# Kernel optimization log

Measured on AMD Instinct MI355X. Metric: run time of the kernel, lower is better.

## Reference

```python
import jax, jax.numpy as jnp
import numpy as np

B, T, IN, EH, GH = 256, 512, 128, 512, 512  # batch, time, channels, enc hidden, gen hidden
UPDATE_BIAS = 1.0
CLIP_VAL = 5.0


def setup_inputs() -> dict:
    key = jax.random.key(0)
    ks = jax.random.split(key, 7)
    s = 0.05  # weight scale to keep gates unsaturated
    return {
        "src": jax.random.normal(ks[0], (B, T, IN), jnp.float32),
        "eps": jax.random.normal(ks[1], (B, GH), jnp.float32),  # reparam noise for generator IC
        "enc_Wi": jax.random.normal(ks[2], (3 * EH, IN), jnp.float32) * s,   # torch GRU weight_ih_l0 (r,z,n)
        "enc_Wh": jax.random.normal(ks[3], (3 * EH, EH), jnp.float32) * s,   # torch GRU weight_hh_l0
        "enc2gen_W": jax.random.normal(ks[4], (2 * GH, EH), jnp.float32) * s,  # Linear enc_state -> ic params
        "gen_Wh_ru": jax.random.normal(ks[5], (2 * GH, GH), jnp.float32) * s,  # GruCellModified fc_h_ru
        "gen_W_rhc": jax.random.normal(ks[6], (GH, GH), jnp.float32) * s,      # GruCellModified fc_rh_c
    }


def _forward(src, eps, enc_Wi, enc_Wh, enc2gen_W, gen_Wh_ru, gen_W_rhc):
    b, t, _ = src.shape
    H = enc_Wh.shape[1]
    # ---- encoder: standard GRU (bias=False), batch_first, 1 layer, unidirectional ----
    xW = jnp.einsum('bti,ki->tbk', src, enc_Wi)  # [T,B,3H], input projections hoisted out of scan

    def enc_step(h, xw):
        gh = h @ enc_Wh.T  # [B,3H]
        xr, xz, xn = jnp.split(xw, 3, axis=-1)
        hr, hz, hn = jnp.split(gh, 3, axis=-1)
        r = jax.nn.sigmoid(xr + hr)
        z = jax.nn.sigmoid(xz + hz)
        n = jnp.tanh(xn + r * hn)
        h_new = (1.0 - z) * n + z * h
        return h_new, None

    h0 = jnp.zeros((b, H), src.dtype)
    enc_last, _ = jax.lax.scan(enc_step, h0, xW)  # [B,EH]

    # ---- enc2gen Linear -> generator IC distribution params ----
    ic_params = enc_last @ enc2gen_W.T  # [B, 2*GH]
    mu, lv = jnp.split(ic_params, 2, axis=1)
    ic = mu + jnp.exp(0.5 * lv) * eps  # reparameterized sample, [B,GH]

    # ---- generator: GruCellModified recurrence, input_size=0 (no input term) ----
    def gen_step(h, _):
        ru = h @ gen_Wh_ru.T  # [B,2*GH]
        r, u = jnp.split(ru, 2, axis=-1)
        r = jax.nn.sigmoid(r)
        u = jax.nn.sigmoid(u + UPDATE_BIAS)  # forced update-gate bias
        c = jnp.tanh((r * h) @ gen_W_rhc.T)
        h_new = u * h + (1.0 - u) * c
        return h_new, h_new

    _, gen_hidden = jax.lax.scan(gen_step, ic, None, length=t)  # [T,B,GH]
    gen_out = jnp.clip(gen_hidden.transpose(1, 0, 2), -CLIP_VAL, CLIP_VAL)  # [B,T,GH]
    return gen_out, ic_params


def reference(src, eps, enc_Wi, enc_Wh, enc2gen_W, gen_Wh_ru, gen_W_rhc):
    return _forward(src, eps, enc_Wi, enc_Wh, enc2gen_W, gen_Wh_ru, gen_W_rhc)
```

## Files before the change

kernel.cpp:

```cpp
#include <hip/hip_runtime.h>
#include <hip/hip_bf16.h>
#include <math.h>

#define BB 256
#define TT 512
#define INW 128
#define EH 512
#define GH 512

#define NGB 32
#define NGRP 8
#define MG 32
#define NB 16

typedef __attribute__((ext_vector_type(8))) short bf16x8;
typedef __attribute__((ext_vector_type(4))) float f32x4;
typedef __attribute__((ext_vector_type(2))) unsigned long long u64x2;

__device__ __forceinline__ float sigm(float x){ return 1.0f/(1.0f+__expf(-x)); }
__device__ __forceinline__ short f2bf(float x){
    __hip_bfloat16 h = __float2bfloat16(x);
    return *reinterpret_cast<short*>(&h);
}

__device__ __forceinline__ unsigned long long ld_coh64(const unsigned long long* p){
    return __hip_atomic_load(p, __ATOMIC_RELAXED, __HIP_MEMORY_SCOPE_AGENT);
}
__device__ __forceinline__ void st_coh32(unsigned* p, unsigned v){
    __hip_atomic_store(p, v, __ATOMIC_RELAXED, __HIP_MEMORY_SCOPE_AGENT);
}

__device__ __forceinline__ void grp_sync(unsigned* cnt, unsigned target) {
    asm volatile("s_waitcnt vmcnt(0)" ::: "memory");
    __syncthreads();
    if (threadIdx.x == 0) {
        __hip_atomic_fetch_add(cnt, 1u, __ATOMIC_RELAXED, __HIP_MEMORY_SCOPE_AGENT);
        long spins = 0;
        while (__hip_atomic_load(cnt, __ATOMIC_RELAXED, __HIP_MEMORY_SCOPE_AGENT) < target) {
            __builtin_amdgcn_s_sleep(1);
            if (++spins > (1L << 22)) break;
        }
    }
    __syncthreads();
}

__device__ __forceinline__ void pack_store_bf(unsigned* dst_even, short bv, int l15){
    unsigned mine = (unsigned short)bv;
    unsigned othr = __shfl_xor(mine, 1);
    if (!(l15 & 1)) st_coh32(dst_even, (othr << 16) | mine);
}

__global__ __launch_bounds__(512, 1) void enc_kernel(
    const float* __restrict__ src,
    const float* __restrict__ Wi,
    const float* __restrict__ Wh,
    short*       __restrict__ hbf,
    float*       __restrict__ hencf,
    unsigned*    __restrict__ bars)
{
    __shared__ __align__(16) char sH[32*1024];
    __shared__ __align__(16) char sX[32*256];
    __shared__ float sR[32*17];
    __shared__ float sZ[32*17];
    __shared__ float sHfp[32*17];

    const int bid = blockIdx.x;
    const int g = bid / NGB, ng = bid % NGB;
    const int tid = threadIdx.x;
    const int wid = tid >> 6, lane = tid & 63;
    const int l15 = lane & 15, lk = lane >> 4;
    const int j0 = ng * NB;
    const int b0 = g * MG;
    unsigned* cnt = bars + g * 32;

    bf16x8 whB[16], wxB[4];
    if (wid < 6) {
        const int gate = wid >> 1;
        const float* wrh = Wh + (size_t)(gate*EH + j0 + l15) * EH;
        const float* wrx = Wi + (size_t)(gate*EH + j0 + l15) * INW;
        #pragma unroll
        for (int kt = 0; kt < 16; ++kt) {
            int ke = kt*32 + lk*8;
            float4 f0 = *(const float4*)(wrh + ke);
            float4 f1 = *(const float4*)(wrh + ke + 4);
            bf16x8 v;
            v[0]=f2bf(f0.x); v[1]=f2bf(f0.y); v[2]=f2bf(f0.z); v[3]=f2bf(f0.w);
            v[4]=f2bf(f1.x); v[5]=f2bf(f1.y); v[6]=f2bf(f1.z); v[7]=f2bf(f1.w);
            whB[kt] = v;
        }
        #pragma unroll
        for (int kt = 0; kt < 4; ++kt) {
            int ke = kt*32 + lk*8;
            float4 f0 = *(const float4*)(wrx + ke);
            float4 f1 = *(const float4*)(wrx + ke + 4);
            bf16x8 v;
            v[0]=f2bf(f0.x); v[1]=f2bf(f0.y); v[2]=f2bf(f0.z); v[3]=f2bf(f0.w);
            v[4]=f2bf(f1.x); v[5]=f2bf(f1.y); v[6]=f2bf(f1.z); v[7]=f2bf(f1.w);
            wxB[kt] = v;
        }
    }
    {
        int row = tid >> 4, col = tid & 15;
        sHfp[row*17 + col] = 0.0f;
    }

    for (int t = 0; t < TT; ++t) {
        const short* hsrc = hbf + (size_t)(t & 1) * BB * EH;
        short*       hdst = hbf + (size_t)((t + 1) & 1) * BB * EH;

        #pragma unroll
        for (int i = 0; i < 4; ++i) {
            int row = i*8 + wid;
            int kb  = lane << 4;
            const unsigned long long* gp =
                (const unsigned long long*)((const char*)(hsrc + (size_t)(b0 + row)*EH) + kb);
            unsigned long long v0 = ld_coh64(gp);
            unsigned long long v1 = ld_coh64(gp + 1);
            u64x2 v; v[0] = v0; v[1] = v1;
            *(u64x2*)(sH + row*1024 + (kb ^ ((row & 7) << 4))) = v;
        }
        {
            int e = tid * 8;
            int row = e >> 7, k = e & 127;
            const float* sp = src + ((size_t)(b0 + row)*TT + t)*INW + k;
            float4 f0 = *(const float4*)sp;
            float4 f1 = *(const float4*)(sp + 4);
            bf16x8 v;
            v[0]=f2bf(f0.x); v[1]=f2bf(f0.y); v[2]=f2bf(f0.z); v[3]=f2bf(f0.w);
            v[4]=f2bf(f1.x); v[5]=f2bf(f1.y); v[6]=f2bf(f1.z); v[7]=f2bf(f1.w);
            int kb = (k*2) ^ ((row & 7) << 4);
            *(bf16x8*)(sX + row*256 + kb) = v;
        }
        __syncthreads();

        f32x4 acch = {0.f,0.f,0.f,0.f};
        f32x4 accx = {0.f,0.f,0.f,0.f};
        const int m = wid & 1;
        if (wid < 6) {
            const int arow = m*16 + l15;
            const int asw  = (arow & 7) << 4;
            const char* hb = sH + arow*1024;
            const char* xb = sX + arow*256;
            #pragma unroll
            for (int kt = 0; kt < 16; ++kt) {
                int kb = kt*64 + lk*16;
                bf16x8 a = *(const bf16x8*)(hb + (kb ^ asw));
                acch = __builtin_amdgcn_mfma_f32_16x16x32_bf16(a, whB[kt], acch, 0, 0, 0);
            }
            #pragma unroll
            for (int kt = 0; kt < 4; ++kt) {
                int kb = kt*64 + lk*16;
                bf16x8 a = *(const bf16x8*)(xb + (kb ^ asw));
                accx = __builtin_amdgcn_mfma_f32_16x16x32_bf16(a, wxB[kt], accx, 0, 0, 0);
            }
        }
        if (wid < 2) {
            #pragma unroll
            for (int v = 0; v < 4; ++v) {
                int row = m*16 + lk*4 + v;
                sR[row*17 + l15] = sigm(accx[v] + acch[v]);
            }
        } else if (wid < 4) {
            #pragma unroll
            for (int v = 0; v < 4; ++v) {
                int row = m*16 + lk*4 + v;
                sZ[row*17 + l15] = sigm(accx[v] + acch[v]);
            }
        }
        __syncthreads();
        if (wid == 4 || wid == 5) {
            #pragma unroll
            for (int v = 0; v < 4; ++v) {
                int row = m*16 + lk*4 + v;
                float r  = sR[row*17 + l15];
                float z  = sZ[row*17 + l15];
                float n  = tanhf(accx[v] + r * acch[v]);
                float hp = sHfp[row*17 + l15];
                float hn = (1.f - z)*n + z*hp;
                sHfp[row*17 + l15] = hn;
                unsigned* dst = (unsigned*)&hdst[(size_t)(b0 + row)*EH + j0 + (l15 & ~1)];
                pack_store_bf(dst, f2bf(hn), l15);
                if (t == TT - 1) hencf[(size_t)(b0 + row)*EH + j0 + l15] = hn;
            }
        }
        grp_sync(cnt, (unsigned)((t + 1) * NGB));
    }
}

__global__ __launch_bounds__(256) void ic_kernel(
    const float* __restrict__ henc,
    const float* __restrict__ W,
    const float* __restrict__ eps,
    float*       __restrict__ out_icp,
    float*       __restrict__ gh0f,
    short*       __restrict__ gh0b)
{
    __shared__ float hb[EH];
    const int b = blockIdx.x, tid = threadIdx.x;
    for (int k = tid; k < EH; k += 256) hb[k] = henc[(size_t)b*EH + k];
    __syncthreads();

    for (int jj = tid; jj < GH; jj += 256) {
        const float4* wm = (const float4*)(W + (size_t)jj * EH);
        const float4* wl = (const float4*)(W + (size_t)(GH + jj) * EH);
        float am = 0.f, al = 0.f;
        #pragma unroll 4
        for (int k4 = 0; k4 < EH/4; ++k4) {
            float4 h = ((const float4*)hb)[k4];
            float4 a = wm[k4], c = wl[k4];
            am += h.x*a.x + h.y*a.y + h.z*a.z + h.w*a.w;
            al += h.x*c.x + h.y*c.y + h.z*c.z + h.w*c.w;
        }
        out_icp[(size_t)b*2*GH + jj]      = am;
        out_icp[(size_t)b*2*GH + GH + jj] = al;
        float icv = am + __expf(0.5f * al) * eps[(size_t)b*GH + jj];
        gh0f[(size_t)b*GH + jj] = icv;
        gh0b[(size_t)b*GH + jj] = f2bf(icv);
    }
}

__global__ __launch_bounds__(512, 1) void gen_kernel(
    const float* __restrict__ Wru,
    const float* __restrict__ Wc,
    const float* __restrict__ gh0f,
    short*       __restrict__ hbf,
    short*       __restrict__ rhbf,
    float*       __restrict__ out,
    unsigned*    __restrict__ bars)
{
    __shared__ __align__(16) char sH[32*1024];
    __shared__ float sU[32*17];
    __shared__ float sHfp[32*17];

    const int bid = blockIdx.x;
    const int g = bid / NGB, ng = bid % NGB;
    const int tid = threadIdx.x;
    const int wid = tid >> 6, lane = tid & 63;
    const int l15 = lane & 15, lk = lane >> 4;
    const int j0 = ng * NB;
    const int b0 = g * MG;
    unsigned* cnt = bars + g * 32;
    short* rhg = rhbf + (size_t)g * MG * GH;

    bf16x8 wB[16];
    if (wid < 6) {
        const float* wr;
        if (wid < 2)      wr = Wru + (size_t)(j0 + l15) * GH;
        else if (wid < 4) wr = Wru + (size_t)(GH + j0 + l15) * GH;
        else              wr = Wc  + (size_t)(j0 + l15) * GH;
        #pragma unroll
        for (int kt = 0; kt < 16; ++kt) {
            int ke = kt*32 + lk*8;
            float4 f0 = *(const float4*)(wr + ke);
            float4 f1 = *(const float4*)(wr + ke + 4);
            bf16x8 v;
            v[0]=f2bf(f0.x); v[1]=f2bf(f0.y); v[2]=f2bf(f0.z); v[3]=f2bf(f0.w);
            v[4]=f2bf(f1.x); v[5]=f2bf(f1.y); v[6]=f2bf(f1.z); v[7]=f2bf(f1.w);
            wB[kt] = v;
        }
    }
    {
        int row = tid >> 4, col = tid & 15;
        sHfp[row*17 + col] = gh0f[(size_t)(b0 + row)*GH + j0 + col];
    }

    for (int t = 0; t < TT; ++t) {
        const short* hsrc = hbf + (size_t)(t & 1) * BB * GH;
        short*       hdst = hbf + (size_t)((t + 1) & 1) * BB * GH;

        #pragma unroll
        for (int i = 0; i < 4; ++i) {
            int row = i*8 + wid;
            int kb  = lane << 4;
            const unsigned long long* gp =
                (const unsigned long long*)((const char*)(hsrc + (size_t)(b0 + row)*GH) + kb);
            unsigned long long v0 = ld_coh64(gp);
            unsigned long long v1 = ld_coh64(gp + 1);
            u64x2 v; v[0] = v0; v[1] = v1;
            *(u64x2*)(sH + row*1024 + (kb ^ ((row & 7) << 4))) = v;
        }
        __syncthreads();

        if (wid < 4) {
            const int m = wid & 1;
            const int arow = m*16 + l15;
            const int asw  = (arow & 7) << 4;
            const char* hb = sH + arow*1024;
            f32x4 acc = {0.f,0.f,0.f,0.f};
            #pragma unroll
            for (int kt = 0; kt < 16; ++kt) {
                int kb = kt*64 + lk*16;
                bf16x8 a = *(const bf16x8*)(hb + (kb ^ asw));
                acc = __builtin_amdgcn_mfma_f32_16x16x32_bf16(a, wB[kt], acc, 0, 0, 0);
            }
            if (wid < 2) {
                #pragma unroll
                for (int v = 0; v < 4; ++v) {
                    int row = m*16 + lk*4 + v;
                    float hp = sHfp[row*17 + l15];
                    float rv = sigm(acc[v]);
                    unsigned* dst = (unsigned*)&rhg[(size_t)row*GH + j0 + (l15 & ~1)];
                    pack_store_bf(dst, f2bf(rv * hp), l15);
                }
            } else {
                #pragma unroll
                for (int v = 0; v < 4; ++v) {
                    int row = m*16 + lk*4 + v;
                    sU[row*17 + l15] = sigm(acc[v] + 1.0f);
                }
            }
        }
        grp_sync(cnt, (unsigned)((2*t + 1) * NGB));

        #pragma unroll
        for (int i = 0; i < 4; ++i) {
            int row = i*8 + wid;
            int kb  = lane << 4;
            const unsigned long long* gp =
                (const unsigned long long*)((const char*)(rhg + (size_t)row*GH) + kb);
            unsigned long long v0 = ld_coh64(gp);
            unsigned long long v1 = ld_coh64(gp + 1);
            u64x2 v; v[0] = v0; v[1] = v1;
            *(u64x2*)(sH + row*1024 + (kb ^ ((row & 7) << 4))) = v;
        }
        __syncthreads();

        if (wid == 4 || wid == 5) {
            const int m = wid & 1;
            const int arow = m*16 + l15;
            const int asw  = (arow & 7) << 4;
            const char* hb = sH + arow*1024;
            f32x4 acc = {0.f,0.f,0.f,0.f};
            #pragma unroll
            for (int kt = 0; kt < 16; ++kt) {
                int kb = kt*64 + lk*16;
                bf16x8 a = *(const bf16x8*)(hb + (kb ^ asw));
                acc = __builtin_amdgcn_mfma_f32_16x16x32_bf16(a, wB[kt], acc, 0, 0, 0);
            }
            #pragma unroll
            for (int v = 0; v < 4; ++v) {
                int row = m*16 + lk*4 + v;
                float cv = tanhf(acc[v]);
                float u  = sU[row*17 + l15];
                float hp = sHfp[row*17 + l15];
                float hn = u*hp + (1.0f - u)*cv;
                sHfp[row*17 + l15] = hn;
                unsigned* dst = (unsigned*)&hdst[(size_t)(b0 + row)*GH + j0 + (l15 & ~1)];
                pack_store_bf(dst, f2bf(hn), l15);
                out[((size_t)(b0 + row)*TT + t)*GH + j0 + l15] = fminf(fmaxf(hn, -5.0f), 5.0f);
            }
        }
        grp_sync(cnt, (unsigned)((2*t + 2) * NGB));
    }
}

extern "C" void kernel_launch(void* const* d_in, const int* in_sizes, int n_in,
                              void* d_out, int out_size, void* d_ws, size_t ws_size,
                              hipStream_t stream) {
    (void)in_sizes; (void)n_in; (void)out_size; (void)ws_size;

    const float* src    = (const float*)d_in[0];
    const float* eps    = (const float*)d_in[1];
    const float* enc_Wi = (const float*)d_in[2];
    const float* enc_Wh = (const float*)d_in[3];
    const float* e2g    = (const float*)d_in[4];
    const float* gWru   = (const float*)d_in[5];
    const float* gWc    = (const float*)d_in[6];
    float* out = (float*)d_out;

    char* ws = (char*)d_ws;
    unsigned* bars = (unsigned*)ws;
    float* hencf = (float*)(ws + 8192);
    float* gh0f  = (float*)(ws + 8192 + 512*1024);
    short* encH  = (short*)(ws + 8192 + 1024*1024);
    short* genH  = (short*)(ws + 8192 + 1536*1024);
    short* rhbf  = (short*)(ws + 8192 + 2048*1024);

    hipMemsetAsync(bars, 0, 8192, stream);
    hipMemsetAsync(encH, 0, (size_t)BB*EH*2, stream);

    enc_kernel<<<dim3(256), dim3(512), 0, stream>>>(src, enc_Wi, enc_Wh, encH, hencf, bars);
    ic_kernel <<<dim3(256), dim3(256), 0, stream>>>(hencf, e2g, eps,
                                                    out + (size_t)BB*TT*GH, gh0f, genH);
    gen_kernel<<<dim3(256), dim3(512), 0, stream>>>(gWru, gWc, gh0f, genH, rhbf, out,
                                                    bars + 1024);
}
```

Before: 5.691 ms.

## Regroup blocks into 16-block groups and use per-block flag barriers

Changes the partition from 8 groups of 32 blocks (32 batch rows, 16 columns each) to 16 groups of 16 blocks (16 batch rows, 32 columns each), so each grid barrier spans fewer blocks and each block loads half as much shared hidden state per step. The atomic-counter barrier is replaced with per-block epoch flags that one wavefront polls in parallel with __all, without sleeping. The MFMA K loop is also split across two accumulators to shorten the dependency chain. The risks are heavier weight-register load per block, busy polling traffic without sleep, and a smaller spin-limit fallback.

```diff
diff --git a/kernel.cpp b/kernel.cpp
--- a/kernel.cpp
+++ b/kernel.cpp
@@ -8,10 +8,11 @@
 #define EH 512
 #define GH 512
 
-#define NGB 32
-#define NGRP 8
-#define MG 32
-#define NB 16
+#define NGRP 16
+#define NGB 16
+#define MG 16
+#define NB 32
+#define FLS 16
 
 typedef __attribute__((ext_vector_type(8))) short bf16x8;
 typedef __attribute__((ext_vector_type(4))) float f32x4;
@@ -30,15 +31,17 @@
     __hip_atomic_store(p, v, __ATOMIC_RELAXED, __HIP_MEMORY_SCOPE_AGENT);
 }
 
-__device__ __forceinline__ void grp_sync(unsigned* cnt, unsigned target) {
+__device__ __forceinline__ void grp_barrier(unsigned* gf, int ng, unsigned e){
     asm volatile("s_waitcnt vmcnt(0)" ::: "memory");
     __syncthreads();
-    if (threadIdx.x == 0) {
-        __hip_atomic_fetch_add(cnt, 1u, __ATOMIC_RELAXED, __HIP_MEMORY_SCOPE_AGENT);
+    if (threadIdx.x == 0) st_coh32(gf + ng*FLS, e);
+    if (threadIdx.x < 64) {
+        const unsigned* p = gf + (threadIdx.x & (NGB-1)) * FLS;
         long spins = 0;
-        while (__hip_atomic_load(cnt, __ATOMIC_RELAXED, __HIP_MEMORY_SCOPE_AGENT) < target) {
-            __builtin_amdgcn_s_sleep(1);
-            if (++spins > (1L << 22)) break;
+        for (;;) {
+            unsigned v = __hip_atomic_load(p, __ATOMIC_RELAXED, __HIP_MEMORY_SCOPE_AGENT);
+            if (__all((int)(v >= e))) break;
+            if (++spins > (1L << 20)) break;
         }
     }
     __syncthreads();
@@ -56,28 +59,29 @@
     const float* __restrict__ Wh,
     short*       __restrict__ hbf,
     float*       __restrict__ hencf,
-    unsigned*    __restrict__ bars)
+    unsigned*    __restrict__ flags)
 {
-    __shared__ __align__(16) char sH[32*1024];
-    __shared__ __align__(16) char sX[32*256];
-    __shared__ float sR[32*17];
-    __shared__ float sZ[32*17];
-    __shared__ float sHfp[32*17];
+    __shared__ __align__(16) char sH[MG*1024];
+    __shared__ __align__(16) char sX[MG*256];
+    __shared__ float sR[MG*33];
+    __shared__ float sZ[MG*33];
+    __shared__ float sHfp[MG*33];
 
     const int bid = blockIdx.x;
-    const int g = bid / NGB, ng = bid % NGB;
+    const int g = bid >> 4, ng = bid & 15;
     const int tid = threadIdx.x;
     const int wid = tid >> 6, lane = tid & 63;
     const int l15 = lane & 15, lk = lane >> 4;
     const int j0 = ng * NB;
     const int b0 = g * MG;
-    unsigned* cnt = bars + g * 32;
+    unsigned* gf = flags + g * NGB * FLS;
 
     bf16x8 whB[16], wxB[4];
+    const int gate = wid >> 1, ct = wid & 1;
+    const int col = ct*16 + l15;
     if (wid < 6) {
-        const int gate = wid >> 1;
-        const float* wrh = Wh + (size_t)(gate*EH + j0 + l15) * EH;
-        const float* wrx = Wi + (size_t)(gate*EH + j0 + l15) * INW;
+        const float* wrh = Wh + (size_t)(gate*EH + j0 + col) * EH;
+        const float* wrx = Wi + (size_t)(gate*EH + j0 + col) * INW;
         #pragma unroll
         for (int kt = 0; kt < 16; ++kt) {
             int ke = kt*32 + lk*8;
@@ -99,19 +103,17 @@
             wxB[kt] = v;
         }
     }
-    {
-        int row = tid >> 4, col = tid & 15;
-        sHfp[row*17 + col] = 0.0f;
-    }
+    sHfp[(tid >> 5)*33 + (tid & 31)] = 0.0f;
 
     for (int t = 0; t < TT; ++t) {
         const short* hsrc = hbf + (size_t)(t & 1) * BB * EH;
         short*       hdst = hbf + (size_t)((t + 1) & 1) * BB * EH;
 
         #pragma unroll
-        for (int i = 0; i < 4; ++i) {
-            int row = i*8 + wid;
-            int kb  = lane << 4;
+        for (int i = 0; i < 2; ++i) {
+            int c = i*512 + tid;
+            int row = c >> 6;
+            int kb  = (c & 63) << 4;
             const unsigned long long* gp =
                 (const unsigned long long*)((const char*)(hsrc + (size_t)(b0 + row)*EH) + kb);
             unsigned long long v0 = ld_coh64(gp);
@@ -119,33 +121,35 @@
             u64x2 v; v[0] = v0; v[1] = v1;
             *(u64x2*)(sH + row*1024 + (kb ^ ((row & 7) << 4))) = v;
         }
-        {
-            int e = tid * 8;
-            int row = e >> 7, k = e & 127;
+        if (tid < 256) {
+            int row = tid >> 4, k = (tid & 15) * 8;
             const float* sp = src + ((size_t)(b0 + row)*TT + t)*INW + k;
             float4 f0 = *(const float4*)sp;
             float4 f1 = *(const float4*)(sp + 4);
             bf16x8 v;
             v[0]=f2bf(f0.x); v[1]=f2bf(f0.y); v[2]=f2bf(f0.z); v[3]=f2bf(f0.w);
             v[4]=f2bf(f1.x); v[5]=f2bf(f1.y); v[6]=f2bf(f1.z); v[7]=f2bf(f1.w);
-            int kb = (k*2) ^ ((row & 7) << 4);
-            *(bf16x8*)(sX + row*256 + kb) = v;
+            *(bf16x8*)(sX + row*256 + ((k*2) ^ ((row & 7) << 4))) = v;
         }
         __syncthreads();
 
-        f32x4 acch = {0.f,0.f,0.f,0.f};
+        f32x4 acc0 = {0.f,0.f,0.f,0.f}, acc1 = {0.f,0.f,0.f,0.f};
         f32x4 accx = {0.f,0.f,0.f,0.f};
-        const int m = wid & 1;
         if (wid < 6) {
-            const int arow = m*16 + l15;
-            const int asw  = (arow & 7) << 4;
-            const char* hb = sH + arow*1024;
-            const char* xb = sX + arow*256;
-            #pragma unroll
-            for (int kt = 0; kt < 16; ++kt) {
-                int kb = kt*64 + lk*16;
-                bf16x8 a = *(const bf16x8*)(hb + (kb ^ asw));
-                acch = __builtin_amdgcn_mfma_f32_16x16x32_bf16(a, whB[kt], acch, 0, 0, 0);
+            const int asw = (l15 & 7) << 4;
+            const char* hb = sH + l15*1024;
+            const char* xb = sX + l15*256;
+            #pragma unroll
+            for (int kt = 0; kt < 8; ++kt) {
+                int kb = kt*64 + lk*16;
+                bf16x8 a = *(const bf16x8*)(hb + (kb ^ asw));
+                acc0 = __builtin_amdgcn_mfma_f32_16x16x32_bf16(a, whB[kt], acc0, 0, 0, 0);
+            }
+            #pragma unroll
+            for (int kt = 8; kt < 16; ++kt) {
+                int kb = kt*64 + lk*16;
+                bf16x8 a = *(const bf16x8*)(hb + (kb ^ asw));
+                acc1 = __builtin_amdgcn_mfma_f32_16x16x32_bf16(a, whB[kt], acc1, 0, 0, 0);
             }
             #pragma unroll
             for (int kt = 0; kt < 4; ++kt) {
@@ -154,36 +158,33 @@
                 accx = __builtin_amdgcn_mfma_f32_16x16x32_bf16(a, wxB[kt], accx, 0, 0, 0);
             }
         }
+        f32x4 acch = acc0 + acc1;
         if (wid < 2) {
             #pragma unroll
-            for (int v = 0; v < 4; ++v) {
-                int row = m*16 + lk*4 + v;
-                sR[row*17 + l15] = sigm(accx[v] + acch[v]);
-            }
+            for (int v = 0; v < 4; ++v)
+                sR[(lk*4 + v)*33 + col] = sigm(accx[v] + acch[v]);
         } else if (wid < 4) {
             #pragma unroll
-            for (int v = 0; v < 4; ++v) {
-                int row = m*16 + lk*4 + v;
-                sZ[row*17 + l15] = sigm(accx[v] + acch[v]);
-            }
+            for (int v = 0; v < 4; ++v)
+                sZ[(lk*4 + v)*33 + col] = sigm(accx[v] + acch[v]);
         }
         __syncthreads();
         if (wid == 4 || wid == 5) {
             #pragma unroll
             for (int v = 0; v < 4; ++v) {
-                int row = m*16 + lk*4 + v;
-                float r  = sR[row*17 + l15];
-                float z  = sZ[row*17 + l15];
+                int row = lk*4 + v;
+                float r  = sR[row*33 + col];
+                float z  = sZ[row*33 + col];
                 float n  = tanhf(accx[v] + r * acch[v]);
-                float hp = sHfp[row*17 + l15];
+                float hp = sHfp[row*33 + col];
                 float hn = (1.f - z)*n + z*hp;
-                sHfp[row*17 + l15] = hn;
-                unsigned* dst = (unsigned*)&hdst[(size_t)(b0 + row)*EH + j0 + (l15 & ~1)];
+                sHfp[row*33 + col] = hn;
+                unsigned* dst = (unsigned*)&hdst[(size_t)(b0 + row)*EH + j0 + ct*16 + (l15 & ~1)];
                 pack_store_bf(dst, f2bf(hn), l15);
-                if (t == TT - 1) hencf[(size_t)(b0 + row)*EH + j0 + l15] = hn;
-            }
-        }
-        grp_sync(cnt, (unsigned)((t + 1) * NGB));
+                if (t == TT - 1) hencf[(size_t)(b0 + row)*EH + j0 + col] = hn;
+            }
+        }
+        grp_barrier(gf, ng, (unsigned)(t + 1));
     }
 }
 
@@ -226,28 +227,30 @@
     short*       __restrict__ hbf,
     short*       __restrict__ rhbf,
     float*       __restrict__ out,
-    unsigned*    __restrict__ bars)
+    unsigned*    __restrict__ flags)
 {
-    __shared__ __align__(16) char sH[32*1024];
-    __shared__ float sU[32*17];
-    __shared__ float sHfp[32*17];
+    __shared__ __align__(16) char sH[MG*1024];
+    __shared__ float sU[MG*33];
+    __shared__ float sHfp[MG*33];
 
     const int bid = blockIdx.x;
-    const int g = bid / NGB, ng = bid % NGB;
+    const int g = bid >> 4, ng = bid & 15;
     const int tid = threadIdx.x;
     const int wid = tid >> 6, lane = tid & 63;
     const int l15 = lane & 15, lk = lane >> 4;
     const int j0 = ng * NB;
     const int b0 = g * MG;
-    unsigned* cnt = bars + g * 32;
+    unsigned* gf = flags + g * NGB * FLS;
     short* rhg = rhbf + (size_t)g * MG * GH;
 
     bf16x8 wB[16];
+    const int gate = wid >> 1, ct = wid & 1;
+    const int col = ct*16 + l15;
     if (wid < 6) {
         const float* wr;
-        if (wid < 2)      wr = Wru + (size_t)(j0 + l15) * GH;
-        else if (wid < 4) wr = Wru + (size_t)(GH + j0 + l15) * GH;
-        else              wr = Wc  + (size_t)(j0 + l15) * GH;
+        if (gate == 0)      wr = Wru + (size_t)(j0 + col) * GH;
+        else if (gate == 1) wr = Wru + (size_t)(GH + j0 + col) * GH;
+        else                wr = Wc  + (size_t)(j0 + col) * GH;
         #pragma unroll
         for (int kt = 0; kt < 16; ++kt) {
             int ke = kt*32 + lk*8;
@@ -260,8 +263,8 @@
         }
     }
     {
-        int row = tid >> 4, col = tid & 15;
-        sHfp[row*17 + col] = gh0f[(size_t)(b0 + row)*GH + j0 + col];
+        int row = tid >> 5, c = tid & 31;
+        sHfp[row*33 + c] = gh0f[(size_t)(b0 + row)*GH + j0 + c];
     }
 
     for (int t = 0; t < TT; ++t) {
@@ -269,9 +272,10 @@
         short*       hdst = hbf + (size_t)((t + 1) & 1) * BB * GH;
 
         #pragma unroll
-        for (int i = 0; i < 4; ++i) {
-            int row = i*8 + wid;
-            int kb  = lane << 4;
+        for (int i = 0; i < 2; ++i) {
+            int c = i*512 + tid;
+            int row = c >> 6;
+            int kb  = (c & 63) << 4;
             const unsigned long long* gp =
                 (const unsigned long long*)((const char*)(hsrc + (size_t)(b0 + row)*GH) + kb);
             unsigned long long v0 = ld_coh64(gp);
@@ -282,40 +286,44 @@
         __syncthreads();
 
         if (wid < 4) {
-            const int m = wid & 1;
-            const int arow = m*16 + l15;
-            const int asw  = (arow & 7) << 4;
-            const char* hb = sH + arow*1024;
-            f32x4 acc = {0.f,0.f,0.f,0.f};
-            #pragma unroll
-            for (int kt = 0; kt < 16; ++kt) {
-                int kb = kt*64 + lk*16;
-                bf16x8 a = *(const bf16x8*)(hb + (kb ^ asw));
-                acc = __builtin_amdgcn_mfma_f32_16x16x32_bf16(a, wB[kt], acc, 0, 0, 0);
-            }
+            const int asw = (l15 & 7) << 4;
+            const char* hb = sH + l15*1024;
+            f32x4 acc0 = {0.f,0.f,0.f,0.f}, acc1 = {0.f,0.f,0.f,0.f};
+            #pragma unroll
+            for (int kt = 0; kt < 8; ++kt) {
+                int kb = kt*64 + lk*16;
+                bf16x8 a = *(const bf16x8*)(hb + (kb ^ asw));
+                acc0 = __builtin_amdgcn_mfma_f32_16x16x32_bf16(a, wB[kt], acc0, 0, 0, 0);
+            }
+            #pragma unroll
+            for (int kt = 8; kt < 16; ++kt) {
+                int kb = kt*64 + lk*16;
+                bf16x8 a = *(const bf16x8*)(hb + (kb ^ asw));
+                acc1 = __builtin_amdgcn_mfma_f32_16x16x32_bf16(a, wB[kt], acc1, 0, 0, 0);
+            }
+            f32x4 acc = acc0 + acc1;
             if (wid < 2) {
                 #pragma unroll
                 for (int v = 0; v < 4; ++v) {
-                    int row = m*16 + lk*4 + v;
-                    float hp = sHfp[row*17 + l15];
+                    int row = lk*4 + v;
+                    float hp = sHfp[row*33 + col];
                     float rv = sigm(acc[v]);
-                    unsigned* dst = (unsigned*)&rhg[(size_t)row*GH + j0 + (l15 & ~1)];
+                    unsigned* dst = (unsigned*)&rhg[(size_t)row*GH + j0 + ct*16 + (l15 & ~1)];
                     pack_store_bf(dst, f2bf(rv * hp), l15);
                 }
             } else {
                 #pragma unroll
-                for (int v = 0; v < 4; ++v) {
-                    int row = m*16 + lk*4 + v;
-                    sU[row*17 + l15] = sigm(acc[v] + 1.0f);
-                }
-            }
-        }
-        grp_sync(cnt, (unsigned)((2*t + 1) * NGB));
-
-        #pragma unroll
-        for (int i = 0; i < 4; ++i) {
-            int row = i*8 + wid;
-            int kb  = lane << 4;
+                for (int v = 0; v < 4; ++v)
+                    sU[(lk*4 + v)*33 + col] = sigm(acc[v] + 1.0f);
+            }
+        }
+        grp_barrier(gf, ng, (unsigned)(2*t + 1));
+
+        #pragma unroll
+        for (int i = 0; i < 2; ++i) {
+            int c = i*512 + tid;
+            int row = c >> 6;
+            int kb  = (c & 63) << 4;
             const unsigned long long* gp =
                 (const unsigned long long*)((const char*)(rhg + (size_t)row*GH) + kb);
             unsigned long long v0 = ld_coh64(gp);
@@ -326,31 +334,36 @@
         __syncthreads();
 
         if (wid == 4 || wid == 5) {
-            const int m = wid & 1;
-            const int arow = m*16 + l15;
-            const int asw  = (arow & 7) << 4;
-            const char* hb = sH + arow*1024;
-            f32x4 acc = {0.f,0.f,0.f,0.f};
-            #pragma unroll
-            for (int kt = 0; kt < 16; ++kt) {
-                int kb = kt*64 + lk*16;
-                bf16x8 a = *(const bf16x8*)(hb + (kb ^ asw));
-                acc = __builtin_amdgcn_mfma_f32_16x16x32_bf16(a, wB[kt], acc, 0, 0, 0);
-            }
+            const int asw = (l15 & 7) << 4;
+            const char* hb = sH + l15*1024;
+            f32x4 acc0 = {0.f,0.f,0.f,0.f}, acc1 = {0.f,0.f,0.f,0.f};
+            #pragma unroll
+            for (int kt = 0; kt < 8; ++kt) {
+                int kb = kt*64 + lk*16;
+                bf16x8 a = *(const bf16x8*)(hb + (kb ^ asw));
+                acc0 = __builtin_amdgcn_mfma_f32_16x16x32_bf16(a, wB[kt], acc0, 0, 0, 0);
+            }
+            #pragma unroll
+            for (int kt = 8; kt < 16; ++kt) {
+                int kb = kt*64 + lk*16;
+                bf16x8 a = *(const bf16x8*)(hb + (kb ^ asw));
+                acc1 = __builtin_amdgcn_mfma_f32_16x16x32_bf16(a, wB[kt], acc1, 0, 0, 0);
+            }
+            f32x4 acc = acc0 + acc1;
             #pragma unroll
             for (int v = 0; v < 4; ++v) {
-                int row = m*16 + lk*4 + v;
+                int row = lk*4 + v;
                 float cv = tanhf(acc[v]);
-                float u  = sU[row*17 + l15];
-                float hp = sHfp[row*17 + l15];
+                float u  = sU[row*33 + col];
+                float hp = sHfp[row*33 + col];
                 float hn = u*hp + (1.0f - u)*cv;
-                sHfp[row*17 + l15] = hn;
-                unsigned* dst = (unsigned*)&hdst[(size_t)(b0 + row)*GH + j0 + (l15 & ~1)];
+                sHfp[row*33 + col] = hn;
+                unsigned* dst = (unsigned*)&hdst[(size_t)(b0 + row)*GH + j0 + ct*16 + (l15 & ~1)];
                 pack_store_bf(dst, f2bf(hn), l15);
-                out[((size_t)(b0 + row)*TT + t)*GH + j0 + l15] = fminf(fmaxf(hn, -5.0f), 5.0f);
-            }
-        }
-        grp_sync(cnt, (unsigned)((2*t + 2) * NGB));
+                out[((size_t)(b0 + row)*TT + t)*GH + j0 + col] = fminf(fmaxf(hn, -5.0f), 5.0f);
+            }
+        }
+        grp_barrier(gf, ng, (unsigned)(2*t + 2));
     }
 }
 
@@ -369,19 +382,20 @@
     float* out = (float*)d_out;
 
     char* ws = (char*)d_ws;
-    unsigned* bars = (unsigned*)ws;
-    float* hencf = (float*)(ws + 8192);
-    float* gh0f  = (float*)(ws + 8192 + 512*1024);
-    short* encH  = (short*)(ws + 8192 + 1024*1024);
-    short* genH  = (short*)(ws + 8192 + 1536*1024);
-    short* rhbf  = (short*)(ws + 8192 + 2048*1024);
-
-    hipMemsetAsync(bars, 0, 8192, stream);
+    unsigned* encFl = (unsigned*)ws;
+    unsigned* genFl = (unsigned*)(ws + 16384);
+    float* hencf = (float*)(ws + 32768);
+    float* gh0f  = (float*)(ws + 32768 + 512*1024);
+    short* encH  = (short*)(ws + 32768 + 1024*1024);
+    short* genH  = (short*)(ws + 32768 + 1536*1024);
+    short* rhbf  = (short*)(ws + 32768 + 2048*1024);
+
+    hipMemsetAsync(ws, 0, 32768, stream);
     hipMemsetAsync(encH, 0, (size_t)BB*EH*2, stream);
 
-    enc_kernel<<<dim3(256), dim3(512), 0, stream>>>(src, enc_Wi, enc_Wh, encH, hencf, bars);
+    enc_kernel<<<dim3(256), dim3(512), 0, stream>>>(src, enc_Wi, enc_Wh, encH, hencf, encFl);
     ic_kernel <<<dim3(256), dim3(256), 0, stream>>>(hencf, e2g, eps,
                                                     out + (size_t)BB*TT*GH, gh0f, genH);
     gen_kernel<<<dim3(256), dim3(512), 0, stream>>>(gWru, gWc, gh0f, genH, rhbf, out,
-                                                    bars + 1024);
-}
+                                                    genFl);
+}
```

New measurement: 4.905 ms. 13.8% less time.
